# Kernel tuning notes

Measured on AMD Instinct MI355X. Metric: run time of the kernel, lower is better.

## Reference

```python
import jax, jax.numpy as jnp
import numpy as np

B, H, L, D = 4, 16, 2048, 64  # batch, heads, seq_len, head_dim


def setup_inputs() -> dict:
    key = jax.random.key(0)
    kq, kk, kv = jax.random.split(key, 3)
    return {
        "query": jax.random.normal(kq, (B, H, L, D), dtype=jnp.float32),
        "key": jax.random.normal(kk, (B, H, L, D), dtype=jnp.float32),
        "value": jax.random.normal(kv, (B, H, L, D), dtype=jnp.float32),
        "mask": jnp.ones((B, L), dtype=jnp.float32),   # unused by the module
        "to_q": jnp.zeros((1,), dtype=jnp.float32),    # unused (pos_emb is None)
        "to_k": jnp.zeros((1,), dtype=jnp.float32),    # unused (pos_emb is None)
    }


def reference(query, key, value, mask, to_q, to_k):
    # pos_emb is None -> no absolute positional transform, no relative bias.
    head_dim = query.shape[-1]
    scale = 1.0 / jnp.sqrt(jnp.asarray(head_dim, dtype=jnp.float32))
    # [b h q d] x [b h k d] -> [b h q k]
    dots = jnp.einsum("bhqd,bhkd->bhqk", query, key) * scale
    attention = jax.nn.softmax(dots, axis=-1)  # dropout prob = 0.0 -> identity
    out = jnp.einsum("bhqk,bhkd->bhqd", attention, value)
    b, h, l, d = out.shape
    # [b h l d] -> [b l h*d]
    return out.transpose(0, 2, 1, 3).reshape(b, l, h * d)
```

## Files before the change

kernel.cpp:

```cpp
#include <hip/hip_runtime.h>

typedef _Float16 f16x8 __attribute__((ext_vector_type(8)));
typedef _Float16 f16x4 __attribute__((ext_vector_type(4)));
typedef _Float16 f16x2 __attribute__((ext_vector_type(2)));
typedef __fp16   h16x2 __attribute__((ext_vector_type(2)));
typedef float    f32x4 __attribute__((ext_vector_type(4)));

static __device__ __forceinline__ f16x2 cvt_pk(float a, float b) {
    h16x2 r = __builtin_amdgcn_cvt_pkrtz(a, b);
    return __builtin_bit_cast(f16x2, r);
}

static __device__ __forceinline__ float fast_exp2(float x) {
#if __has_builtin(__builtin_amdgcn_exp2f)
    return __builtin_amdgcn_exp2f(x);
#else
    float r;
    asm("v_exp_f32 %0, %1" : "=v"(r) : "v"(x));
    return r;
#endif
}

namespace {
constexpr int kH = 16, kL = 2048, kD = 64;
constexpr int QBLK   = 128;
constexpr int KVBLK  = 32;
constexpr int NCHUNK = kL / KVBLK;
constexpr size_t TILE_BYTES = (size_t)KVBLK * kD * 2;
}

#define GLL16(g, l) __builtin_amdgcn_global_load_lds( \
    (const __attribute__((address_space(1))) unsigned int*)(g), \
    (__attribute__((address_space(3))) unsigned int*)(l), 16, 0, 0)

__global__ __launch_bounds__(256, 8)
void prep_kv(const float* __restrict__ K, const float* __restrict__ V,
             _Float16* __restrict__ K16, _Float16* __restrict__ V16)
{
    __shared__ uint4 tile4[512];
    char* tileb = (char*)tile4;
    const int tid = threadIdx.x;
    int blk = blockIdx.x;
    if (blk < 2048) {
        const float4* src = (const float4*)(K + (size_t)blk * 64 * kD);
        char* dst = (char*)K16 + (size_t)blk * 8192;
        #pragma unroll
        for (int i = 0; i < 4; ++i) {
            int f = tid + i * 256;
            int row = f >> 4, c4 = f & 15;
            int tile = row >> 5, r = row & 31;
            float4 v = src[f];
            f16x4 hv = {(_Float16)v.x, (_Float16)v.y, (_Float16)v.z, (_Float16)v.w};
            *(f16x4*)(dst + tile*4096 + r*128 + ((c4*8) ^ ((r & 7) << 4))) = hv;
        }
    } else {
        blk -= 2048;
        const float* vsrc = V + (size_t)blk * 64 * kD;
        int tr = tid >> 4, tc = tid & 15;
        float4 rv[4];
        #pragma unroll
        for (int j = 0; j < 4; ++j)
            rv[j] = *(const float4*)(vsrc + (size_t)(tr*4 + j) * kD + tc*4);
        int tile = tr >> 3, trl = tr & 7;
        int slot = trl & 3;
        int bit3 = ((trl >> 2) & 1) << 3;
        #pragma unroll
        for (int cj = 0; cj < 4; ++cj) {
            int row = tc*4 + cj;
            f16x4 hv = { (_Float16)((&rv[0].x)[cj]), (_Float16)((&rv[1].x)[cj]),
                         (_Float16)((&rv[2].x)[cj]), (_Float16)((&rv[3].x)[cj]) };
            int byte = tile*4096 + row*64 + ((slot ^ ((row >> 1) & 3)) << 4) + bit3;
            *(f16x4*)(tileb + byte) = hv;
        }
        __syncthreads();
        uint4* out = (uint4*)((char*)V16 + (size_t)blk * 8192);
        out[tid]       = tile4[tid];
        out[tid + 256] = tile4[tid + 256];
    }
}

__global__ __launch_bounds__(256, 4)
void attn_fwd(const float* __restrict__ Qg, const _Float16* __restrict__ K16,
              const _Float16* __restrict__ V16, float* __restrict__ Og)
{
    __shared__ uint4 sb4[4][512];

    const int tid  = threadIdx.x;
    const int wv   = tid >> 6;
    const int lane = tid & 63;
    const int lo   = lane & 15;
    const int hi   = lane >> 4;
    const int rsw   = (lo & 7) << 4;
    const int koff0 = (hi * 16) ^ rsw;
    const int koff1 = (64 + hi * 16) ^ rsw;
    const int voff  = ((hi ^ ((lo >> 1) & 3)) << 4);
    const int lo128 = lo * 128;
    const int lo64  = lo * 64;

    const int blk  = blockIdx.x;
    const int bh   = (blk & 7) * 8 + (blk >> 7);
    const int qt   = (blk >> 3) & 15;
    const int q0   = qt * QBLK;
    const int b    = bh >> 4;
    const int h    = bh & 15;

    const float QS = 0.125f * 1.44269504088896340736f;

    f16x8 qf[2][2];
    #pragma unroll
    for (int g = 0; g < 2; ++g) {
        const float* qb = Qg + ((size_t)bh * kL + (q0 + wv*32 + g*16 + lo)) * kD;
        #pragma unroll
        for (int s = 0; s < 2; ++s) {
            const float* p = qb + s*32 + hi*8;
            float4 a0 = *(const float4*)(p);
            float4 a1 = *(const float4*)(p + 4);
            f16x8 q;
            q[0] = (_Float16)(a0.x * QS); q[1] = (_Float16)(a0.y * QS);
            q[2] = (_Float16)(a0.z * QS); q[3] = (_Float16)(a0.w * QS);
            q[4] = (_Float16)(a1.x * QS); q[5] = (_Float16)(a1.y * QS);
            q[6] = (_Float16)(a1.z * QS); q[7] = (_Float16)(a1.w * QS);
            qf[g][s] = q;
        }
    }

    f32x4 acc[2][4];
    #pragma unroll
    for (int g = 0; g < 2; ++g)
        #pragma unroll
        for (int dt = 0; dt < 4; ++dt) acc[g][dt] = (f32x4){0.f, 0.f, 0.f, 0.f};
    float mrow[2] = {-1e30f, -1e30f};
    float lrow[2] = {0.f, 0.f};

    const char* kptr = (const char*)K16 + (size_t)bh * NCHUNK * TILE_BYTES + wv*1024 + lane*16;
    const char* vptr = (const char*)V16 + (size_t)bh * NCHUNK * TILE_BYTES + wv*1024 + lane*16;

    auto stage = [&](int bufi) {
        GLL16(kptr, (char*)sb4[bufi] + wv*1024);
        GLL16(vptr, (char*)sb4[bufi] + 4096 + wv*1024);
        kptr += TILE_BYTES;
        vptr += TILE_BYTES;
    };

    stage(0); stage(1); stage(2);

    for (int t = 0; t < NCHUNK; ++t) {
        if (t <= NCHUNK - 3)      asm volatile("s_waitcnt vmcnt(4)" ::: "memory");
        else if (t == NCHUNK - 2) asm volatile("s_waitcnt vmcnt(2)" ::: "memory");
        else                      asm volatile("s_waitcnt vmcnt(0)" ::: "memory");
        __builtin_amdgcn_s_barrier();
        if (t + 3 < NCHUNK) stage((t + 3) & 3);

        const char* sK = (const char*)sb4[t & 3];
        const char* sV = (const char*)sb4[t & 3] + 4096;

        f32x4 s4[2][2];
        s4[0][0] = (f32x4){0.f,0.f,0.f,0.f}; s4[0][1] = (f32x4){0.f,0.f,0.f,0.f};
        s4[1][0] = (f32x4){0.f,0.f,0.f,0.f}; s4[1][1] = (f32x4){0.f,0.f,0.f,0.f};
        {
            f16x8 kf00 = *(const f16x8*)(sK + lo128 + koff0);
            f16x8 kf10 = *(const f16x8*)(sK + 2048 + lo128 + koff0);
            s4[0][0] = __builtin_amdgcn_mfma_f32_16x16x32_f16(kf00, qf[0][0], s4[0][0], 0, 0, 0);
            s4[1][0] = __builtin_amdgcn_mfma_f32_16x16x32_f16(kf00, qf[1][0], s4[1][0], 0, 0, 0);
            s4[0][1] = __builtin_amdgcn_mfma_f32_16x16x32_f16(kf10, qf[0][0], s4[0][1], 0, 0, 0);
            s4[1][1] = __builtin_amdgcn_mfma_f32_16x16x32_f16(kf10, qf[1][0], s4[1][1], 0, 0, 0);
            f16x8 kf01 = *(const f16x8*)(sK + lo128 + koff1);
            f16x8 kf11 = *(const f16x8*)(sK + 2048 + lo128 + koff1);
            s4[0][0] = __builtin_amdgcn_mfma_f32_16x16x32_f16(kf01, qf[0][1], s4[0][0], 0, 0, 0);
            s4[1][0] = __builtin_amdgcn_mfma_f32_16x16x32_f16(kf01, qf[1][1], s4[1][0], 0, 0, 0);
            s4[0][1] = __builtin_amdgcn_mfma_f32_16x16x32_f16(kf11, qf[0][1], s4[0][1], 0, 0, 0);
            s4[1][1] = __builtin_amdgcn_mfma_f32_16x16x32_f16(kf11, qf[1][1], s4[1][1], 0, 0, 0);
        }

        f16x8 vf0 = *(const f16x8*)(sV +        lo64 + voff);
        f16x8 vf1 = *(const f16x8*)(sV + 1024 + lo64 + voff);
        f16x8 vf2 = *(const f16x8*)(sV + 2048 + lo64 + voff);
        f16x8 vf3 = *(const f16x8*)(sV + 3072 + lo64 + voff);

        f16x8 pf[2];
        #pragma unroll
        for (int g = 0; g < 2; ++g) {
            float mx = fmaxf(fmaxf(fmaxf(s4[g][0][0], s4[g][0][1]), fmaxf(s4[g][0][2], s4[g][0][3])),
                             fmaxf(fmaxf(s4[g][1][0], s4[g][1][1]), fmaxf(s4[g][1][2], s4[g][1][3])));
            if (!__all(mx <= mrow[g] + 8.f)) {
                mx = fmaxf(mx, __shfl_xor(mx, 16));
                mx = fmaxf(mx, __shfl_xor(mx, 32));
                float mnew = fmaxf(mrow[g], mx);
                float al = fast_exp2(mrow[g] - mnew);
                mrow[g] = mnew;
                lrow[g] *= al;
                float a0 = __shfl(al, hi*4 + 0);
                float a1 = __shfl(al, hi*4 + 1);
                float a2 = __shfl(al, hi*4 + 2);
                float a3 = __shfl(al, hi*4 + 3);
                #pragma unroll
                for (int dt = 0; dt < 4; ++dt) {
                    acc[g][dt][0] *= a0; acc[g][dt][1] *= a1;
                    acc[g][dt][2] *= a2; acc[g][dt][3] *= a3;
                }
            }
            float ps = 0.f;
            #pragma unroll
            for (int nt = 0; nt < 2; ++nt)
                #pragma unroll
                for (int r = 0; r < 4; ++r) {
                    float p = fast_exp2(s4[g][nt][r] - mrow[g]);
                    s4[g][nt][r] = p;
                    ps += p;
                }
            lrow[g] += ps;
            f16x2 c0 = cvt_pk(s4[g][0][0], s4[g][0][1]);
            f16x2 c1 = cvt_pk(s4[g][0][2], s4[g][0][3]);
            f16x2 c2 = cvt_pk(s4[g][1][0], s4[g][1][1]);
            f16x2 c3 = cvt_pk(s4[g][1][2], s4[g][1][3]);
            f16x8 p = {c0[0], c0[1], c1[0], c1[1], c2[0], c2[1], c3[0], c3[1]};
            pf[g] = p;
        }

        acc[0][0] = __builtin_amdgcn_mfma_f32_16x16x32_f16(pf[0], vf0, acc[0][0], 0, 0, 0);
        acc[1][0] = __builtin_amdgcn_mfma_f32_16x16x32_f16(pf[1], vf0, acc[1][0], 0, 0, 0);
        acc[0][1] = __builtin_amdgcn_mfma_f32_16x16x32_f16(pf[0], vf1, acc[0][1], 0, 0, 0);
        acc[1][1] = __builtin_amdgcn_mfma_f32_16x16x32_f16(pf[1], vf1, acc[1][1], 0, 0, 0);
        acc[0][2] = __builtin_amdgcn_mfma_f32_16x16x32_f16(pf[0], vf2, acc[0][2], 0, 0, 0);
        acc[1][2] = __builtin_amdgcn_mfma_f32_16x16x32_f16(pf[1], vf2, acc[1][2], 0, 0, 0);
        acc[0][3] = __builtin_amdgcn_mfma_f32_16x16x32_f16(pf[0], vf3, acc[0][3], 0, 0, 0);
        acc[1][3] = __builtin_amdgcn_mfma_f32_16x16x32_f16(pf[1], vf3, acc[1][3], 0, 0, 0);
    }

    #pragma unroll
    for (int g = 0; g < 2; ++g) {
        float l = lrow[g];
        l += __shfl_xor(l, 16);
        l += __shfl_xor(l, 32);
        float linv = 1.f / l;
        float i0 = __shfl(linv, hi*4 + 0);
        float i1 = __shfl(linv, hi*4 + 1);
        float i2 = __shfl(linv, hi*4 + 2);
        float i3 = __shfl(linv, hi*4 + 3);
        #pragma unroll
        for (int dt = 0; dt < 4; ++dt) {
            int col = h*kD + dt*16 + lo;
            int rb  = q0 + wv*32 + g*16 + hi*4;
            Og[((size_t)b * kL + (rb + 0)) * (kH * kD) + col] = acc[g][dt][0] * i0;
            Og[((size_t)b * kL + (rb + 1)) * (kH * kD) + col] = acc[g][dt][1] * i1;
            Og[((size_t)b * kL + (rb + 2)) * (kH * kD) + col] = acc[g][dt][2] * i2;
            Og[((size_t)b * kL + (rb + 3)) * (kH * kD) + col] = acc[g][dt][3] * i3;
        }
    }
}

__global__ __launch_bounds__(256, 4)
void attn_fwd_fb(const float* __restrict__ Qg, const float* __restrict__ Kg,
                 const float* __restrict__ Vg, float* __restrict__ Og)
{
    __shared__ _Float16 sK[64][64];
    __shared__ _Float16 sV[64][64];

    const int tid  = threadIdx.x;
    const int wv   = tid >> 6;
    const int lane = tid & 63;
    const int lo   = lane & 15;
    const int hi   = lane >> 4;

    const int blk  = blockIdx.x;
    const int bh   = (blk & 7) * 8 + (blk >> 7);
    const int qt   = (blk >> 3) & 15;
    const int q0   = qt * 128;
    const int b    = bh >> 4;
    const int h    = bh & 15;

    const float QS = 0.125f * 1.44269504088896340736f;

    f16x8 qf[2][2];
    #pragma unroll
    for (int g = 0; g < 2; ++g) {
        const float* qb = Qg + ((size_t)bh * kL + (q0 + wv*32 + g*16 + lo)) * kD;
        #pragma unroll
        for (int s = 0; s < 2; ++s) {
            const float* p = qb + s*32 + hi*8;
            float4 a0 = *(const float4*)(p);
            float4 a1 = *(const float4*)(p + 4);
            f16x8 q;
            q[0] = (_Float16)(a0.x * QS); q[1] = (_Float16)(a0.y * QS);
            q[2] = (_Float16)(a0.z * QS); q[3] = (_Float16)(a0.w * QS);
            q[4] = (_Float16)(a1.x * QS); q[5] = (_Float16)(a1.y * QS);
            q[6] = (_Float16)(a1.z * QS); q[7] = (_Float16)(a1.w * QS);
            qf[g][s] = q;
        }
    }

    f32x4 acc[2][4];
    #pragma unroll
    for (int g = 0; g < 2; ++g)
        #pragma unroll
        for (int dt = 0; dt < 4; ++dt) acc[g][dt] = (f32x4){0.f, 0.f, 0.f, 0.f};

    float mrow[2] = {-1e30f, -1e30f};
    float lrow[2] = {0.f, 0.f};

    const float* kb = Kg + (size_t)bh * kL * kD;
    const float* vb = Vg + (size_t)bh * kL * kD;

    for (int kv = 0; kv < kL; kv += 64) {
        __syncthreads();
        {
            const float4* src = (const float4*)(kb + (size_t)kv * kD);
            #pragma unroll
            for (int i = 0; i < 4; ++i) {
                int f   = tid + i * 256;
                int row = f >> 4;
                int c4  = f & 15;
                float4 v = src[f];
                f16x4 hv = {(_Float16)v.x, (_Float16)v.y, (_Float16)v.z, (_Float16)v.w};
                int bo = (c4 * 8) ^ ((row & 7) << 4);
                *(f16x4*)((char*)&sK[row][0] + bo) = hv;
            }
        }
        {
            const float* vsrc = vb + (size_t)kv * kD;
            int tr = tid >> 4;
            int tc = tid & 15;
            float4 rv[4];
            #pragma unroll
            for (int j = 0; j < 4; ++j)
                rv[j] = *(const float4*)(vsrc + (size_t)(tr*4 + j) * kD + tc*4);
            int posbyte = ((tr >> 3) << 6) + ((tr & 3) << 4) + (((tr >> 2) & 1) << 3);
            #pragma unroll
            for (int cj = 0; cj < 4; ++cj) {
                int row = tc * 4 + cj;
                f16x4 hv = { (_Float16)((&rv[0].x)[cj]), (_Float16)((&rv[1].x)[cj]),
                             (_Float16)((&rv[2].x)[cj]), (_Float16)((&rv[3].x)[cj]) };
                int bo = posbyte ^ ((row & 7) << 4);
                *(f16x4*)((char*)&sV[row][0] + bo) = hv;
            }
        }
        __syncthreads();

        f16x8 vfrag[2][4];
        #pragma unroll
        for (int kkt = 0; kkt < 2; ++kkt)
            #pragma unroll
            for (int dt = 0; dt < 4; ++dt) {
                int row = dt*16 + lo;
                int bo = (kkt*64 + hi*16) ^ ((row & 7) << 4);
                vfrag[kkt][dt] = *(const f16x8*)((const char*)&sV[row][0] + bo);
            }

        #pragma unroll
        for (int g = 0; g < 2; ++g) {
            f32x4 s4[4];
            #pragma unroll
            for (int nt = 0; nt < 4; ++nt) s4[nt] = (f32x4){0.f, 0.f, 0.f, 0.f};
            #pragma unroll
            for (int ks = 0; ks < 2; ++ks)
                #pragma unroll
                for (int nt = 0; nt < 4; ++nt) {
                    int row = nt*16 + lo;
                    int bo = (ks*64 + hi*16) ^ ((row & 7) << 4);
                    f16x8 kf = *(const f16x8*)((const char*)&sK[row][0] + bo);
                    s4[nt] = __builtin_amdgcn_mfma_f32_16x16x32_f16(kf, qf[g][ks], s4[nt], 0, 0, 0);
                }
            float mx = fmaxf(fmaxf(s4[0][0], s4[0][1]), fmaxf(s4[0][2], s4[0][3]));
            #pragma unroll
            for (int nt = 1; nt < 4; ++nt)
                mx = fmaxf(mx, fmaxf(fmaxf(s4[nt][0], s4[nt][1]), fmaxf(s4[nt][2], s4[nt][3])));
            mx = fmaxf(mx, __shfl_xor(mx, 16));
            mx = fmaxf(mx, __shfl_xor(mx, 32));
            float mnew = fmaxf(mrow[g], mx);
            float al = fast_exp2(mrow[g] - mnew);
            mrow[g] = mnew;
            float ps = 0.f;
            #pragma unroll
            for (int nt = 0; nt < 4; ++nt)
                #pragma unroll
                for (int r = 0; r < 4; ++r) {
                    float p = fast_exp2(s4[nt][r] - mnew);
                    s4[nt][r] = p;
                    ps += p;
                }
            ps += __shfl_xor(ps, 16);
            ps += __shfl_xor(ps, 32);
            lrow[g] = lrow[g] * al + ps;
            f16x8 pf[2];
            #pragma unroll
            for (int kkt = 0; kkt < 2; ++kkt) {
                f16x8 p;
                p[0] = (_Float16)s4[2*kkt][0];   p[1] = (_Float16)s4[2*kkt][1];
                p[2] = (_Float16)s4[2*kkt][2];   p[3] = (_Float16)s4[2*kkt][3];
                p[4] = (_Float16)s4[2*kkt+1][0]; p[5] = (_Float16)s4[2*kkt+1][1];
                p[6] = (_Float16)s4[2*kkt+1][2]; p[7] = (_Float16)s4[2*kkt+1][3];
                pf[kkt] = p;
            }
            float a0 = __shfl(al, hi*4 + 0);
            float a1 = __shfl(al, hi*4 + 1);
            float a2 = __shfl(al, hi*4 + 2);
            float a3 = __shfl(al, hi*4 + 3);
            #pragma unroll
            for (int dt = 0; dt < 4; ++dt) {
                acc[g][dt][0] *= a0; acc[g][dt][1] *= a1;
                acc[g][dt][2] *= a2; acc[g][dt][3] *= a3;
            }
            #pragma unroll
            for (int kkt = 0; kkt < 2; ++kkt)
                #pragma unroll
                for (int dt = 0; dt < 4; ++dt)
                    acc[g][dt] = __builtin_amdgcn_mfma_f32_16x16x32_f16(pf[kkt], vfrag[kkt][dt], acc[g][dt], 0, 0, 0);
        }
    }

    #pragma unroll
    for (int g = 0; g < 2; ++g) {
        float linv = 1.f / lrow[g];
        float i0 = __shfl(linv, hi*4 + 0);
        float i1 = __shfl(linv, hi*4 + 1);
        float i2 = __shfl(linv, hi*4 + 2);
        float i3 = __shfl(linv, hi*4 + 3);
        #pragma unroll
        for (int dt = 0; dt < 4; ++dt) {
            int col = h*kD + dt*16 + lo;
            int rb  = q0 + wv*32 + g*16 + hi*4;
            Og[((size_t)b * kL + (rb + 0)) * (kH * kD) + col] = acc[g][dt][0] * i0;
            Og[((size_t)b * kL + (rb + 1)) * (kH * kD) + col] = acc[g][dt][1] * i1;
            Og[((size_t)b * kL + (rb + 2)) * (kH * kD) + col] = acc[g][dt][2] * i2;
            Og[((size_t)b * kL + (rb + 3)) * (kH * kD) + col] = acc[g][dt][3] * i3;
        }
    }
}

extern "C" void kernel_launch(void* const* d_in, const int* in_sizes, int n_in,
                              void* d_out, int out_size, void* d_ws, size_t ws_size,
                              hipStream_t stream) {
    const float* Qg = (const float*)d_in[0];
    const float* Kg = (const float*)d_in[1];
    const float* Vg = (const float*)d_in[2];
    float* Og = (float*)d_out;

    const size_t imgElems = (size_t)64 * kL * kD;
    if (ws_size >= imgElems * 2 * sizeof(_Float16)) {
        _Float16* K16 = (_Float16*)d_ws;
        _Float16* V16 = K16 + imgElems;
        prep_kv<<<dim3(4096), dim3(256), 0, stream>>>(Kg, Vg, K16, V16);
        attn_fwd<<<dim3(1024), dim3(256), 0, stream>>>(Qg, K16, V16, Og);
    } else {
        attn_fwd_fb<<<dim3(1024), dim3(256), 0, stream>>>(Qg, Kg, Vg, Og);
    }
}
```

Before: 111.6 us.

## Fold max subtraction into MFMA init, unroll loop by 4, sum probabilities via fdot2

The score accumulators now start at -mrow, so the MFMA produces max-subtracted logits directly. This removes the per-element subtraction before exp2 and turns the rescale check into a fixed threshold. The main loop is unrolled by four with constant buffer indices and an explicit epilogue, which drops the per-iteration branching on vmcnt and the dynamic buffer selection. Row sums are now taken from the packed fp16 probabilities using fdot2 instead of fp32 adds, so lrow matches the rounded values fed to the PV MFMA but is accumulated in fewer instructions.

After: 105.1 us. 5.8% less time.

```diff
diff --git a/kernel.cpp b/kernel.cpp
--- a/kernel.cpp
+++ b/kernel.cpp
@@ -18,6 +18,15 @@
     float r;
     asm("v_exp_f32 %0, %1" : "=v"(r) : "v"(x));
     return r;
+#endif
+}
+
+static __device__ __forceinline__ float pairsum(f16x2 a, float c) {
+#if __has_builtin(__builtin_amdgcn_fdot2)
+    h16x2 one = {(__fp16)1.f, (__fp16)1.f};
+    return __builtin_amdgcn_fdot2(__builtin_bit_cast(h16x2, a), one, c, false);
+#else
+    return c + (float)a[0] + (float)a[1];
 #endif
 }
 
@@ -129,7 +138,7 @@
     for (int g = 0; g < 2; ++g)
         #pragma unroll
         for (int dt = 0; dt < 4; ++dt) acc[g][dt] = (f32x4){0.f, 0.f, 0.f, 0.f};
-    float mrow[2] = {-1e30f, -1e30f};
+    float mrow[2] = {0.f, 0.f};
     float lrow[2] = {0.f, 0.f};
 
     const char* kptr = (const char*)K16 + (size_t)bh * NCHUNK * TILE_BYTES + wv*1024 + lane*16;
@@ -142,21 +151,17 @@
         vptr += TILE_BYTES;
     };
 
-    stage(0); stage(1); stage(2);
-
-    for (int t = 0; t < NCHUNK; ++t) {
-        if (t <= NCHUNK - 3)      asm volatile("s_waitcnt vmcnt(4)" ::: "memory");
-        else if (t == NCHUNK - 2) asm volatile("s_waitcnt vmcnt(2)" ::: "memory");
-        else                      asm volatile("s_waitcnt vmcnt(0)" ::: "memory");
-        __builtin_amdgcn_s_barrier();
-        if (t + 3 < NCHUNK) stage((t + 3) & 3);
-
-        const char* sK = (const char*)sb4[t & 3];
-        const char* sV = (const char*)sb4[t & 3] + 4096;
+    auto tile = [&](int J) {
+        const char* sK = (const char*)sb4[J];
+        const char* sV = sK + 4096;
 
         f32x4 s4[2][2];
-        s4[0][0] = (f32x4){0.f,0.f,0.f,0.f}; s4[0][1] = (f32x4){0.f,0.f,0.f,0.f};
-        s4[1][0] = (f32x4){0.f,0.f,0.f,0.f}; s4[1][1] = (f32x4){0.f,0.f,0.f,0.f};
+        #pragma unroll
+        for (int g = 0; g < 2; ++g) {
+            float nm = -mrow[g];
+            f32x4 mi = {nm, nm, nm, nm};
+            s4[g][0] = mi; s4[g][1] = mi;
+        }
         {
             f16x8 kf00 = *(const f16x8*)(sK + lo128 + koff0);
             f16x8 kf10 = *(const f16x8*)(sK + 2048 + lo128 + koff0);
@@ -182,12 +187,12 @@
         for (int g = 0; g < 2; ++g) {
             float mx = fmaxf(fmaxf(fmaxf(s4[g][0][0], s4[g][0][1]), fmaxf(s4[g][0][2], s4[g][0][3])),
                              fmaxf(fmaxf(s4[g][1][0], s4[g][1][1]), fmaxf(s4[g][1][2], s4[g][1][3])));
-            if (!__all(mx <= mrow[g] + 8.f)) {
+            if (!__all(mx <= 8.f)) {
                 mx = fmaxf(mx, __shfl_xor(mx, 16));
                 mx = fmaxf(mx, __shfl_xor(mx, 32));
-                float mnew = fmaxf(mrow[g], mx);
-                float al = fast_exp2(mrow[g] - mnew);
-                mrow[g] = mnew;
+                float d  = fmaxf(mx, 0.f);
+                float al = fast_exp2(-d);
+                mrow[g] += d;
                 lrow[g] *= al;
                 float a0 = __shfl(al, hi*4 + 0);
                 float a1 = __shfl(al, hi*4 + 1);
@@ -198,21 +203,21 @@
                     acc[g][dt][0] *= a0; acc[g][dt][1] *= a1;
                     acc[g][dt][2] *= a2; acc[g][dt][3] *= a3;
                 }
-            }
-            float ps = 0.f;
+                #pragma unroll
+                for (int nt = 0; nt < 2; ++nt)
+                    #pragma unroll
+                    for (int r = 0; r < 4; ++r) s4[g][nt][r] -= d;
+            }
             #pragma unroll
             for (int nt = 0; nt < 2; ++nt)
                 #pragma unroll
-                for (int r = 0; r < 4; ++r) {
-                    float p = fast_exp2(s4[g][nt][r] - mrow[g]);
-                    s4[g][nt][r] = p;
-                    ps += p;
-                }
-            lrow[g] += ps;
+                for (int r = 0; r < 4; ++r)
+                    s4[g][nt][r] = fast_exp2(s4[g][nt][r]);
             f16x2 c0 = cvt_pk(s4[g][0][0], s4[g][0][1]);
             f16x2 c1 = cvt_pk(s4[g][0][2], s4[g][0][3]);
             f16x2 c2 = cvt_pk(s4[g][1][0], s4[g][1][1]);
             f16x2 c3 = cvt_pk(s4[g][1][2], s4[g][1][3]);
+            lrow[g] += pairsum(c0, pairsum(c1, pairsum(c2, pairsum(c3, 0.f))));
             f16x8 p = {c0[0], c0[1], c1[0], c1[1], c2[0], c2[1], c3[0], c3[1]};
             pf[g] = p;
         }
@@ -225,7 +230,32 @@
         acc[1][2] = __builtin_amdgcn_mfma_f32_16x16x32_f16(pf[1], vf2, acc[1][2], 0, 0, 0);
         acc[0][3] = __builtin_amdgcn_mfma_f32_16x16x32_f16(pf[0], vf3, acc[0][3], 0, 0, 0);
         acc[1][3] = __builtin_amdgcn_mfma_f32_16x16x32_f16(pf[1], vf3, acc[1][3], 0, 0, 0);
-    }
+    };
+
+    stage(0); stage(1); stage(2);
+
+    for (int tt = 0; tt < NCHUNK - 4; tt += 4) {
+        #pragma unroll
+        for (int j = 0; j < 4; ++j) {
+            asm volatile("s_waitcnt vmcnt(4)" ::: "memory");
+            __builtin_amdgcn_s_barrier();
+            stage((j + 3) & 3);
+            tile(j);
+        }
+    }
+    asm volatile("s_waitcnt vmcnt(4)" ::: "memory");
+    __builtin_amdgcn_s_barrier();
+    stage(3);
+    tile(0);
+    asm volatile("s_waitcnt vmcnt(4)" ::: "memory");
+    __builtin_amdgcn_s_barrier();
+    tile(1);
+    asm volatile("s_waitcnt vmcnt(2)" ::: "memory");
+    __builtin_amdgcn_s_barrier();
+    tile(2);
+    asm volatile("s_waitcnt vmcnt(0)" ::: "memory");
+    __builtin_amdgcn_s_barrier();
+    tile(3);
 
     #pragma unroll
     for (int g = 0; g < 2; ++g) {
```
